# Kernel tuning notes

Measured on AMD Instinct MI355X. Metric: run time of the kernel, lower is better.

The kernel has to match this reference:

```python
import jax, jax.numpy as jnp
import numpy as np

P = 8            # window_size
SHIFT = P // 2   # cyclic shift for 'SW' type
HEADS = 6        # input_dim // head_dim = 192 // 32
HD = 32          # head_dim
C = 192          # input_dim
OUT = 192        # output_dim
SCALE = HD ** (-0.5)


def setup_inputs() -> dict:
    key = jax.random.key(0)
    ks = jax.random.split(key, 8)
    f = lambda k, sh: jax.random.normal(k, sh, dtype=jnp.float32)
    return {
        "x": f(ks[0], (2, 256, 256, C)),
        "b": f(ks[1], (2, 256, 256, C)),
        "w_qkv": f(ks[2], (3 * C, C)) * 0.02,
        "b_qkv": jnp.zeros((3 * C,), jnp.float32),
        "w_qkv_b": f(ks[3], (3 * C, C)) * 0.02,
        "b_qkv_b": jnp.zeros((3 * C,), jnp.float32),
        "rel_params": f(ks[4], (HEADS, 2 * P - 1, 2 * P - 1)) * 0.02,
        "w_out": f(ks[5], (OUT, C)) * 0.02,
        "b_out": jnp.zeros((OUT,), jnp.float32),
    }


def _rel_bias(rel_params):
    # gathered relative position bias: (HEADS, P*P, P*P)
    cord = np.array([[i, j] for i in range(P) for j in range(P)])
    rel = cord[:, None, :] - cord[None, :, :] + P - 1
    return rel_params[:, rel[:, :, 0], rel[:, :, 1]]


def _shift_mask(hw, ww):
    # bool mask (nw, P*P, P*P); True -> -inf before softmax
    m = np.zeros((hw, ww, P, P, P, P), dtype=bool)
    s = P - SHIFT
    m[-1, :, :s, :, s:, :] = True
    m[-1, :, s:, :, :s, :] = True
    m[:, -1, :, :s, :, s:] = True
    m[:, -1, :, s:, :, :s] = True
    return jnp.asarray(m.reshape(hw * ww, P * P, P * P))


def reference(x, b, w_qkv, b_qkv, w_qkv_b, b_qkv_b, rel_params, w_out, b_out):
    # cyclic shift (type != 'W')
    x = jnp.roll(x, (-SHIFT, -SHIFT), axis=(1, 2))
    b = jnp.roll(b, (-SHIFT, -SHIFT), axis=(1, 2))
    B, H, W, c = x.shape
    hw, ww = H // P, W // P
    nw, pp = hw * ww, P * P

    def windows(t):  # [B,H,W,C] -> [B,nw,pp,C]
        return t.reshape(B, hw, P, ww, P, c).transpose(0, 1, 3, 2, 4, 5).reshape(B, nw, pp, c)

    xw, bw = windows(x), windows(b)

    def qkv(t, w, bb):  # returns q,k,v each (HEADS, B, nw, pp, HD)
        e = (t @ w.T + bb).reshape(B, nw, pp, 3 * HEADS, HD)
        e = jnp.moveaxis(e, 3, 0)
        return e[:HEADS], e[HEADS:2 * HEADS], e[2 * HEADS:]

    _, k, v = qkv(xw, w_qkv, b_qkv)
    q_b, _, _ = qkv(bw, w_qkv_b, b_qkv_b)

    sim = jnp.einsum('hbwpc,hbwqc->hbwpq', q_b, k) * SCALE
    sim = sim + _rel_bias(rel_params)[:, None, None]
    mask = _shift_mask(hw, ww)  # (nw, pp, pp)
    sim = jnp.where(mask[None, None], -jnp.inf, sim)
    probs = jax.nn.softmax(sim, axis=-1)
    out = jnp.einsum('hbwij,hbwjc->hbwic', probs, v)
    out = jnp.moveaxis(out, 0, 3).reshape(B, nw, pp, HEADS * HD)
    out = out @ w_out.T + b_out
    out = out.reshape(B, hw, ww, P, P, OUT).transpose(0, 1, 3, 2, 4, 5).reshape(B, H, W, OUT)
    return jnp.roll(out, (SHIFT, SHIFT), axis=(1, 2))
```

## Files before the change

### kernel.cpp

```cpp
#include <hip/hip_runtime.h>


#define NHEADS 6
#define CDIM 192
#define IMG 256
#define SHIFTV 4
#define SCALE_F 0.17677669529663687f

typedef __attribute__((ext_vector_type(8))) _Float16 h8;
typedef __attribute__((ext_vector_type(4))) _Float16 h4;
typedef __attribute__((ext_vector_type(4))) float f4;

#define MFMA(a, b, c) __builtin_amdgcn_mfma_f32_16x16x32_f16((a), (b), (c), 0, 0, 0)

__global__ void prep_weights(const float* __restrict__ wqb,
                             const float* __restrict__ wqkv,
                             const float* __restrict__ wout,
                             _Float16* __restrict__ dst)
{
    const int i = blockIdx.x * 256 + threadIdx.x;
    const int m = i / 36864, r = i - m * 36864;
    float v;
    if (m == 0)      v = wqb[r];
    else if (m == 1) v = wqkv[36864 + r];
    else if (m == 2) v = wqkv[73728 + r];
    else             v = wout[r];
    dst[i] = (_Float16)v;
}

__global__ void prep_table(const float* __restrict__ rel, float* __restrict__ tab)
{
    const int i = blockIdx.x * 256 + threadIdx.x;
    const int k = i & 63, q = (i >> 6) & 63;
    const int th = i >> 12;
    const int h = th % 6, ty = th / 6;
    const int pr = q >> 3, pc = q & 7, qr = k >> 3, qc = k & 7;
    const bool msk = ((ty & 1) && ((pr < 4) != (qr < 4))) ||
                     ((ty & 2) && ((pc < 4) != (qc < 4)));
    const float bias = rel[h * 225 + (pr - qr + 7) * 15 + (pc - qc + 7)];
    tab[i] = msk ? -1e30f : bias;
}

__global__ __launch_bounds__(256, 3)
void wmca_mfma(const float* __restrict__ x, const float* __restrict__ bten,
               const float* __restrict__ b_qkv, const float* __restrict__ b_qkv_b,
               const float* __restrict__ b_out,
               const _Float16* __restrict__ wh, const float* __restrict__ tab,
               float* __restrict__ out)
{
    __shared__ _Float16 sX[64 * 200];
    __shared__ _Float16 sQ[64 * 40];
    __shared__ _Float16 sK[64 * 40];
    __shared__ _Float16 sVt[32 * 72];
    __shared__ _Float16 sP[64 * 72];

    const int t = threadIdx.x;
    const int w = t >> 6, l = t & 63, g = l >> 4, c16 = l & 15;

    const int wid = blockIdx.x;
    const int bi = wid >> 10, whi = (wid >> 5) & 31, wwi = wid & 31;
    const int ty = ((whi == 31) ? 1 : 0) | ((wwi == 31) ? 2 : 0);

    {
        const int rr = t >> 2, part = t & 3;
        const int pr = rr >> 3, pc = rr & 7;
        const int ho = (whi * 8 + pr + SHIFTV) & 255;
        const int wo = (wwi * 8 + pc + SHIFTV) & 255;
        const float4* xs = (const float4*)(x + ((bi * IMG + ho) * IMG + wo) * CDIM);
        _Float16* dX = sX + rr * 200;
#pragma unroll
        for (int i = 0; i < 12; ++i) {
            const int q4 = part + 4 * i;
            const float4 v = xs[q4];
            h4 hv; hv[0] = (_Float16)v.x; hv[1] = (_Float16)v.y;
                   hv[2] = (_Float16)v.z; hv[3] = (_Float16)v.w;
            *(h4*)(dX + 4 * q4) = hv;
        }
    }

    const int tokA = 16 * w + c16;
    const int prA = tokA >> 3, pcA = tokA & 7;
    const int hoA = (whi * 8 + prA + SHIFTV) & 255;
    const int woA = (wwi * 8 + pcA + SHIFTV) & 255;
    const float* bA = bten + ((bi * IMG + hoA) * IMG + woA) * CDIM;

    h8 aQ[6];
#pragma unroll
    for (int ks = 0; ks < 6; ++ks) {
        const float4 f0 = *(const float4*)(bA + ks * 32 + 8 * g);
        const float4 f1 = *(const float4*)(bA + ks * 32 + 8 * g + 4);
        h8 a;
        a[0] = (_Float16)f0.x; a[1] = (_Float16)f0.y;
        a[2] = (_Float16)f0.z; a[3] = (_Float16)f0.w;
        a[4] = (_Float16)f1.x; a[5] = (_Float16)f1.y;
        a[6] = (_Float16)f1.z; a[7] = (_Float16)f1.w;
        aQ[ks] = a;
    }

    f4 pacc[12];
#pragma unroll
    for (int nt = 0; nt < 12; ++nt) {
        const float bo = b_out[16 * nt + c16];
        pacc[nt] = (f4){bo, bo, bo, bo};
    }

    const _Float16* Wq = wh;
    const _Float16* Wk = wh + 36864;
    const _Float16* Wv = wh + 2 * 36864;
    const _Float16* Wo = wh + 3 * 36864;
    const int vm = w & 1, vn = w >> 1;

    __syncthreads();

    for (int h = 0; h < NHEADS; ++h) {
        {
            const float b0 = b_qkv_b[h * 32 + c16];
            const float b1 = b_qkv_b[h * 32 + 16 + c16];
            f4 a0 = {b0, b0, b0, b0}, a1 = {b1, b1, b1, b1};
            const _Float16* wr0 = Wq + (h * 32 + c16) * 192 + 8 * g;
            const _Float16* wr1 = wr0 + 16 * 192;
#pragma unroll
            for (int ks = 0; ks < 6; ++ks) {
                a0 = MFMA(aQ[ks], *(const h8*)(wr0 + ks * 32), a0);
                a1 = MFMA(aQ[ks], *(const h8*)(wr1 + ks * 32), a1);
            }
#pragma unroll
            for (int rg = 0; rg < 4; ++rg) {
                sQ[(16 * w + 4 * g + rg) * 40 + c16]      = (_Float16)(a0[rg] * SCALE_F);
                sQ[(16 * w + 4 * g + rg) * 40 + 16 + c16] = (_Float16)(a1[rg] * SCALE_F);
            }
        }
        {
            const float b0 = b_qkv[CDIM + h * 32 + c16];
            const float b1 = b_qkv[CDIM + h * 32 + 16 + c16];
            f4 a0 = {b0, b0, b0, b0}, a1 = {b1, b1, b1, b1};
            const _Float16* xr = sX + (16 * w + c16) * 200 + 8 * g;
            const _Float16* wr0 = Wk + (h * 32 + c16) * 192 + 8 * g;
            const _Float16* wr1 = wr0 + 16 * 192;
#pragma unroll
            for (int ks = 0; ks < 6; ++ks) {
                const h8 a = *(const h8*)(xr + ks * 32);
                a0 = MFMA(a, *(const h8*)(wr0 + ks * 32), a0);
                a1 = MFMA(a, *(const h8*)(wr1 + ks * 32), a1);
            }
#pragma unroll
            for (int rg = 0; rg < 4; ++rg) {
                sK[(16 * w + 4 * g + rg) * 40 + c16]      = (_Float16)a0[rg];
                sK[(16 * w + 4 * g + rg) * 40 + 16 + c16] = (_Float16)a1[rg];
            }
        }
        {
            const float4 bv = *(const float4*)(b_qkv + 2 * CDIM + h * 32 + 16 * vm + 4 * g);
            f4 a0 = {bv.x, bv.y, bv.z, bv.w};
            f4 a1 = a0;
            const _Float16* wr = Wv + (h * 32 + 16 * vm + c16) * 192 + 8 * g;
            const _Float16* x0 = sX + (32 * vn + c16) * 200 + 8 * g;
            const _Float16* x1 = x0 + 16 * 200;
#pragma unroll
            for (int ks = 0; ks < 6; ++ks) {
                const h8 a = *(const h8*)(wr + ks * 32);
                a0 = MFMA(a, *(const h8*)(x0 + ks * 32), a0);
                a1 = MFMA(a, *(const h8*)(x1 + ks * 32), a1);
            }
#pragma unroll
            for (int rg = 0; rg < 4; ++rg) {
                sVt[(16 * vm + 4 * g + rg) * 72 + 32 * vn + c16]      = (_Float16)a0[rg];
                sVt[(16 * vm + 4 * g + rg) * 72 + 32 * vn + 16 + c16] = (_Float16)a1[rg];
            }
        }
        __syncthreads();

        {
            const float* tr = tab + ((ty * 6 + h) << 12) + (16 * w + 4 * g) * 64 + c16;
            f4 s0, s1, s2, s3;
#pragma unroll
            for (int rg = 0; rg < 4; ++rg) {
                s0[rg] = tr[rg * 64];
                s1[rg] = tr[rg * 64 + 16];
                s2[rg] = tr[rg * 64 + 32];
                s3[rg] = tr[rg * 64 + 48];
            }
            const h8 qa = *(const h8*)(sQ + (16 * w + c16) * 40 + 8 * g);
            s0 = MFMA(qa, *(const h8*)(sK + c16 * 40 + 8 * g), s0);
            s1 = MFMA(qa, *(const h8*)(sK + (16 + c16) * 40 + 8 * g), s1);
            s2 = MFMA(qa, *(const h8*)(sK + (32 + c16) * 40 + 8 * g), s2);
            s3 = MFMA(qa, *(const h8*)(sK + (48 + c16) * 40 + 8 * g), s3);
#pragma unroll
            for (int rg = 0; rg < 4; ++rg) {
                float mx = fmaxf(fmaxf(s0[rg], s1[rg]), fmaxf(s2[rg], s3[rg]));
                mx = fmaxf(mx, __shfl_xor(mx, 1));
                mx = fmaxf(mx, __shfl_xor(mx, 2));
                mx = fmaxf(mx, __shfl_xor(mx, 4));
                mx = fmaxf(mx, __shfl_xor(mx, 8));
                const float e0 = __expf(s0[rg] - mx);
                const float e1 = __expf(s1[rg] - mx);
                const float e2 = __expf(s2[rg] - mx);
                const float e3 = __expf(s3[rg] - mx);
                float sm = e0 + e1 + e2 + e3;
                sm += __shfl_xor(sm, 1);
                sm += __shfl_xor(sm, 2);
                sm += __shfl_xor(sm, 4);
                sm += __shfl_xor(sm, 8);
                const float inv = 1.0f / sm;
                _Float16* prow = sP + (16 * w + 4 * g + rg) * 72 + c16;
                prow[0]  = (_Float16)(e0 * inv);
                prow[16] = (_Float16)(e1 * inv);
                prow[32] = (_Float16)(e2 * inv);
                prow[48] = (_Float16)(e3 * inv);
            }
        }

        {
            const h8 pa0 = *(const h8*)(sP + (16 * w + c16) * 72 + 8 * g);
            const h8 pa1 = *(const h8*)(sP + (16 * w + c16) * 72 + 32 + 8 * g);
            f4 o0 = {0.f, 0.f, 0.f, 0.f}, o1 = o0;
            o0 = MFMA(pa0, *(const h8*)(sVt + c16 * 72 + 8 * g), o0);
            o0 = MFMA(pa1, *(const h8*)(sVt + c16 * 72 + 32 + 8 * g), o0);
            o1 = MFMA(pa0, *(const h8*)(sVt + (16 + c16) * 72 + 8 * g), o1);
            o1 = MFMA(pa1, *(const h8*)(sVt + (16 + c16) * 72 + 32 + 8 * g), o1);
#pragma unroll
            for (int rg = 0; rg < 4; ++rg) {
                sQ[(16 * w + 4 * g + rg) * 40 + c16]      = (_Float16)o0[rg];
                sQ[(16 * w + 4 * g + rg) * 40 + 16 + c16] = (_Float16)o1[rg];
            }
        }
        __syncthreads();

        {
            const h8 oa = *(const h8*)(sQ + (16 * w + c16) * 40 + 8 * g);
            const _Float16* wr = Wo + c16 * 192 + h * 32 + 8 * g;
#pragma unroll
            for (int nt = 0; nt < 12; ++nt)
                pacc[nt] = MFMA(oa, *(const h8*)(wr + nt * 16 * 192), pacc[nt]);
        }
    }

#pragma unroll
    for (int rg = 0; rg < 4; ++rg) {
        const int token = 16 * w + 4 * g + rg;
        const int pr = token >> 3, pc = token & 7;
        const int ho = (whi * 8 + pr + SHIFTV) & 255;
        const int wo = (wwi * 8 + pc + SHIFTV) & 255;
        float* po = out + ((bi * IMG + ho) * IMG + wo) * CDIM + c16;
#pragma unroll
        for (int nt = 0; nt < 12; ++nt)
            po[16 * nt] = pacc[nt][rg];
    }
}

extern "C" void kernel_launch(void* const* d_in, const int* in_sizes, int n_in,
                              void* d_out, int out_size, void* d_ws, size_t ws_size,
                              hipStream_t stream)
{
    const float* x       = (const float*)d_in[0];
    const float* b       = (const float*)d_in[1];
    const float* w_qkv   = (const float*)d_in[2];
    const float* b_qkv   = (const float*)d_in[3];
    const float* w_qkv_b = (const float*)d_in[4];
    const float* b_qkv_b = (const float*)d_in[5];
    const float* rel     = (const float*)d_in[6];
    const float* w_out   = (const float*)d_in[7];
    const float* b_out   = (const float*)d_in[8];
    float* out = (float*)d_out;

    _Float16* wh = (_Float16*)d_ws;
    float* tab = (float*)((char*)d_ws + 294912);

    prep_weights<<<576, 256, 0, stream>>>(w_qkv_b, w_qkv, w_out, wh);
    prep_table<<<384, 256, 0, stream>>>(rel, tab);
    wmca_mfma<<<2048, 256, 0, stream>>>(x, b, b_qkv, b_qkv_b, b_out, wh, tab, out);
}
```

Before: 514.2 us.

## Assign one wavefront per head and drop per-head block barriers

```diff
diff --git a/kernel.cpp b/kernel.cpp
--- a/kernel.cpp
+++ b/kernel.cpp
@@ -1,17 +1,26 @@
 #include <hip/hip_runtime.h>
 
 
-#define NHEADS 6
-#define CDIM 192
 #define IMG 256
 #define SHIFTV 4
 #define SCALE_F 0.17677669529663687f
 
 typedef __attribute__((ext_vector_type(8))) _Float16 h8;
-typedef __attribute__((ext_vector_type(4))) _Float16 h4;
 typedef __attribute__((ext_vector_type(4))) float f4;
 
 #define MFMA(a, b, c) __builtin_amdgcn_mfma_f32_16x16x32_f16((a), (b), (c), 0, 0, 0)
+
+__device__ __forceinline__ h8 cvt8(const float* __restrict__ p)
+{
+    const float4 f0 = *(const float4*)p;
+    const float4 f1 = *(const float4*)(p + 4);
+    h8 a;
+    a[0] = (_Float16)f0.x; a[1] = (_Float16)f0.y;
+    a[2] = (_Float16)f0.z; a[3] = (_Float16)f0.w;
+    a[4] = (_Float16)f1.x; a[5] = (_Float16)f1.y;
+    a[6] = (_Float16)f1.z; a[7] = (_Float16)f1.w;
+    return a;
+}
 
 __global__ void prep_weights(const float* __restrict__ wqb,
                              const float* __restrict__ wqkv,
@@ -41,211 +50,261 @@
     tab[i] = msk ? -1e30f : bias;
 }
 
-__global__ __launch_bounds__(256, 3)
-void wmca_mfma(const float* __restrict__ x, const float* __restrict__ bten,
-               const float* __restrict__ b_qkv, const float* __restrict__ b_qkv_b,
-               const float* __restrict__ b_out,
-               const _Float16* __restrict__ wh, const float* __restrict__ tab,
-               float* __restrict__ out)
-{
-    __shared__ _Float16 sX[64 * 200];
-    __shared__ _Float16 sQ[64 * 40];
-    __shared__ _Float16 sK[64 * 40];
-    __shared__ _Float16 sVt[32 * 72];
-    __shared__ _Float16 sP[64 * 72];
+__global__ __launch_bounds__(384, 3)
+void wmca_hpw(const float* __restrict__ x, const float* __restrict__ bten,
+              const float* __restrict__ b_qkv, const float* __restrict__ b_qkv_b,
+              const float* __restrict__ b_out,
+              const _Float16* __restrict__ wh, const float* __restrict__ tab,
+              float* __restrict__ out)
+{
+    __shared__ _Float16 sPool[6 * 64 * 72];
 
     const int t = threadIdx.x;
-    const int w = t >> 6, l = t & 63, g = l >> 4, c16 = l & 15;
+    const int w = t >> 6;
+    const int l = t & 63, g = l >> 4, c16 = l & 15;
 
     const int wid = blockIdx.x;
     const int bi = wid >> 10, whi = (wid >> 5) & 31, wwi = wid & 31;
     const int ty = ((whi == 31) ? 1 : 0) | ((wwi == 31) ? 2 : 0);
 
-    {
-        const int rr = t >> 2, part = t & 3;
-        const int pr = rr >> 3, pc = rr & 7;
-        const int ho = (whi * 8 + pr + SHIFTV) & 255;
-        const int wo = (wwi * 8 + pc + SHIFTV) & 255;
-        const float4* xs = (const float4*)(x + ((bi * IMG + ho) * IMG + wo) * CDIM);
-        _Float16* dX = sX + rr * 200;
-#pragma unroll
-        for (int i = 0; i < 12; ++i) {
-            const int q4 = part + 4 * i;
-            const float4 v = xs[q4];
-            h4 hv; hv[0] = (_Float16)v.x; hv[1] = (_Float16)v.y;
-                   hv[2] = (_Float16)v.z; hv[3] = (_Float16)v.w;
-            *(h4*)(dX + 4 * q4) = hv;
-        }
-    }
-
-    const int tokA = 16 * w + c16;
-    const int prA = tokA >> 3, pcA = tokA & 7;
-    const int hoA = (whi * 8 + prA + SHIFTV) & 255;
-    const int woA = (wwi * 8 + pcA + SHIFTV) & 255;
-    const float* bA = bten + ((bi * IMG + hoA) * IMG + woA) * CDIM;
-
-    h8 aQ[6];
-#pragma unroll
-    for (int ks = 0; ks < 6; ++ks) {
-        const float4 f0 = *(const float4*)(bA + ks * 32 + 8 * g);
-        const float4 f1 = *(const float4*)(bA + ks * 32 + 8 * g + 4);
-        h8 a;
-        a[0] = (_Float16)f0.x; a[1] = (_Float16)f0.y;
-        a[2] = (_Float16)f0.z; a[3] = (_Float16)f0.w;
-        a[4] = (_Float16)f1.x; a[5] = (_Float16)f1.y;
-        a[6] = (_Float16)f1.z; a[7] = (_Float16)f1.w;
-        aQ[ks] = a;
-    }
-
-    f4 pacc[12];
-#pragma unroll
-    for (int nt = 0; nt < 12; ++nt) {
-        const float bo = b_out[16 * nt + c16];
-        pacc[nt] = (f4){bo, bo, bo, bo};
+    _Float16* bounce = sPool + w * (64 * 72);
+
+    const float* xR[4]; const float* bR[4];
+#pragma unroll
+    for (int m = 0; m < 4; ++m) {
+        const int tok = 16 * m + c16;
+        const int ho = (whi * 8 + (tok >> 3) + SHIFTV) & 255;
+        const int wo = (wwi * 8 + (tok & 7) + SHIFTV) & 255;
+        const int base = ((bi * IMG + ho) * IMG + wo) * 192;
+        xR[m] = x + base; bR[m] = bten + base;
     }
 
     const _Float16* Wq = wh;
     const _Float16* Wk = wh + 36864;
     const _Float16* Wv = wh + 2 * 36864;
     const _Float16* Wo = wh + 3 * 36864;
-    const int vm = w & 1, vn = w >> 1;
+
+    {
+        f4 qacc[4][2];
+#pragma unroll
+        for (int n = 0; n < 2; ++n) {
+            const float bb = b_qkv_b[w * 32 + 16 * n + c16];
+#pragma unroll
+            for (int m = 0; m < 4; ++m) qacc[m][n] = (f4){bb, bb, bb, bb};
+        }
+#pragma unroll
+        for (int ks = 0; ks < 6; ++ks) {
+            h8 wB0 = *(const h8*)(Wq + (w * 32 + c16) * 192 + 32 * ks + 8 * g);
+            h8 wB1 = *(const h8*)(Wq + (w * 32 + 16 + c16) * 192 + 32 * ks + 8 * g);
+#pragma unroll
+            for (int m = 0; m < 4; ++m) {
+                const h8 aB = cvt8(bR[m] + 32 * ks + 8 * g);
+                qacc[m][0] = MFMA(aB, wB0, qacc[m][0]);
+                qacc[m][1] = MFMA(aB, wB1, qacc[m][1]);
+            }
+        }
+#pragma unroll
+        for (int m = 0; m < 4; ++m)
+#pragma unroll
+            for (int n = 0; n < 2; ++n)
+#pragma unroll
+                for (int rg = 0; rg < 4; ++rg)
+                    bounce[(16 * m + 4 * g + rg) * 72 + 16 * n + c16] =
+                        (_Float16)(qacc[m][n][rg] * SCALE_F);
+    }
+    h8 qa[4];
+#pragma unroll
+    for (int m = 0; m < 4; ++m)
+        qa[m] = *(const h8*)(bounce + (16 * m + c16) * 72 + 8 * g);
+
+    {
+        f4 kacc[4][2];
+#pragma unroll
+        for (int n = 0; n < 2; ++n) {
+            const float bb = b_qkv[192 + w * 32 + 16 * n + c16];
+#pragma unroll
+            for (int m = 0; m < 4; ++m) kacc[m][n] = (f4){bb, bb, bb, bb};
+        }
+#pragma unroll
+        for (int ks = 0; ks < 6; ++ks) {
+            h8 wB0 = *(const h8*)(Wk + (w * 32 + c16) * 192 + 32 * ks + 8 * g);
+            h8 wB1 = *(const h8*)(Wk + (w * 32 + 16 + c16) * 192 + 32 * ks + 8 * g);
+#pragma unroll
+            for (int m = 0; m < 4; ++m) {
+                const h8 aB = cvt8(xR[m] + 32 * ks + 8 * g);
+                kacc[m][0] = MFMA(aB, wB0, kacc[m][0]);
+                kacc[m][1] = MFMA(aB, wB1, kacc[m][1]);
+            }
+        }
+#pragma unroll
+        for (int m = 0; m < 4; ++m)
+#pragma unroll
+            for (int n = 0; n < 2; ++n)
+#pragma unroll
+                for (int rg = 0; rg < 4; ++rg)
+                    bounce[(16 * m + 4 * g + rg) * 72 + 16 * n + c16] =
+                        (_Float16)kacc[m][n][rg];
+    }
+    h8 kb[4];
+#pragma unroll
+    for (int n = 0; n < 4; ++n)
+        kb[n] = *(const h8*)(bounce + (16 * n + c16) * 72 + 8 * g);
+
+    {
+        f4 vacc[2][4];
+#pragma unroll
+        for (int mv = 0; mv < 2; ++mv) {
+            const float4 bv = *(const float4*)(b_qkv + 384 + w * 32 + 16 * mv + 4 * g);
+#pragma unroll
+            for (int n = 0; n < 4; ++n) vacc[mv][n] = (f4){bv.x, bv.y, bv.z, bv.w};
+        }
+#pragma unroll
+        for (int ks = 0; ks < 6; ++ks) {
+            h8 wA0 = *(const h8*)(Wv + (w * 32 + c16) * 192 + 32 * ks + 8 * g);
+            h8 wA1 = *(const h8*)(Wv + (w * 32 + 16 + c16) * 192 + 32 * ks + 8 * g);
+#pragma unroll
+            for (int n = 0; n < 4; ++n) {
+                const h8 xv = cvt8(xR[n] + 32 * ks + 8 * g);
+                vacc[0][n] = MFMA(wA0, xv, vacc[0][n]);
+                vacc[1][n] = MFMA(wA1, xv, vacc[1][n]);
+            }
+        }
+#pragma unroll
+        for (int mv = 0; mv < 2; ++mv)
+#pragma unroll
+            for (int n = 0; n < 4; ++n)
+#pragma unroll
+                for (int rg = 0; rg < 4; ++rg)
+                    bounce[(16 * mv + 4 * g + rg) * 72 + 16 * n + c16] =
+                        (_Float16)vacc[mv][n][rg];
+    }
+    h8 vb[2][2];
+#pragma unroll
+    for (int ks2 = 0; ks2 < 2; ++ks2)
+#pragma unroll
+        for (int n = 0; n < 2; ++n)
+            vb[ks2][n] = *(const h8*)(bounce + (16 * n + c16) * 72 + 32 * ks2 + 8 * g);
+
+    f4 s[4][4];
+    {
+        const float* tb = tab + ((ty * 6 + w) << 12);
+#pragma unroll
+        for (int m = 0; m < 4; ++m)
+#pragma unroll
+            for (int n = 0; n < 4; ++n)
+#pragma unroll
+                for (int rg = 0; rg < 4; ++rg)
+                    s[m][n][rg] = tb[(16 * m + 4 * g + rg) * 64 + 16 * n + c16];
+#pragma unroll
+        for (int m = 0; m < 4; ++m)
+#pragma unroll
+            for (int n = 0; n < 4; ++n)
+                s[m][n] = MFMA(qa[m], kb[n], s[m][n]);
+    }
+
+    f4 inv4[4];
+#pragma unroll
+    for (int m = 0; m < 4; ++m) {
+#pragma unroll
+        for (int rg = 0; rg < 4; ++rg) {
+            float mx = fmaxf(fmaxf(s[m][0][rg], s[m][1][rg]),
+                             fmaxf(s[m][2][rg], s[m][3][rg]));
+            mx = fmaxf(mx, __shfl_xor(mx, 1));
+            mx = fmaxf(mx, __shfl_xor(mx, 2));
+            mx = fmaxf(mx, __shfl_xor(mx, 4));
+            mx = fmaxf(mx, __shfl_xor(mx, 8));
+            const float e0 = __expf(s[m][0][rg] - mx);
+            const float e1 = __expf(s[m][1][rg] - mx);
+            const float e2 = __expf(s[m][2][rg] - mx);
+            const float e3 = __expf(s[m][3][rg] - mx);
+            float sm = e0 + e1 + e2 + e3;
+            sm += __shfl_xor(sm, 1);
+            sm += __shfl_xor(sm, 2);
+            sm += __shfl_xor(sm, 4);
+            sm += __shfl_xor(sm, 8);
+            inv4[m][rg] = 1.0f / sm;
+            _Float16* prow = bounce + (16 * m + 4 * g + rg) * 72 + c16;
+            prow[0]  = (_Float16)e0;
+            prow[16] = (_Float16)e1;
+            prow[32] = (_Float16)e2;
+            prow[48] = (_Float16)e3;
+        }
+    }
+
+    f4 o[4][2];
+    {
+        h8 pa[4][2];
+#pragma unroll
+        for (int m = 0; m < 4; ++m)
+#pragma unroll
+            for (int ks2 = 0; ks2 < 2; ++ks2)
+                pa[m][ks2] = *(const h8*)(bounce + (16 * m + c16) * 72 + 32 * ks2 + 8 * g);
+#pragma unroll
+        for (int m = 0; m < 4; ++m)
+#pragma unroll
+            for (int n = 0; n < 2; ++n) {
+                f4 acc = (f4){0.f, 0.f, 0.f, 0.f};
+                acc = MFMA(pa[m][0], vb[0][n], acc);
+                acc = MFMA(pa[m][1], vb[1][n], acc);
+                o[m][n] = acc;
+            }
+#pragma unroll
+        for (int m = 0; m < 4; ++m)
+#pragma unroll
+            for (int n = 0; n < 2; ++n)
+#pragma unroll
+                for (int rg = 0; rg < 4; ++rg)
+                    o[m][n][rg] *= inv4[m][rg];
+    }
 
     __syncthreads();
 
-    for (int h = 0; h < NHEADS; ++h) {
-        {
-            const float b0 = b_qkv_b[h * 32 + c16];
-            const float b1 = b_qkv_b[h * 32 + 16 + c16];
-            f4 a0 = {b0, b0, b0, b0}, a1 = {b1, b1, b1, b1};
-            const _Float16* wr0 = Wq + (h * 32 + c16) * 192 + 8 * g;
-            const _Float16* wr1 = wr0 + 16 * 192;
-#pragma unroll
-            for (int ks = 0; ks < 6; ++ks) {
-                a0 = MFMA(aQ[ks], *(const h8*)(wr0 + ks * 32), a0);
-                a1 = MFMA(aQ[ks], *(const h8*)(wr1 + ks * 32), a1);
-            }
-#pragma unroll
-            for (int rg = 0; rg < 4; ++rg) {
-                sQ[(16 * w + 4 * g + rg) * 40 + c16]      = (_Float16)(a0[rg] * SCALE_F);
-                sQ[(16 * w + 4 * g + rg) * 40 + 16 + c16] = (_Float16)(a1[rg] * SCALE_F);
-            }
-        }
-        {
-            const float b0 = b_qkv[CDIM + h * 32 + c16];
-            const float b1 = b_qkv[CDIM + h * 32 + 16 + c16];
-            f4 a0 = {b0, b0, b0, b0}, a1 = {b1, b1, b1, b1};
-            const _Float16* xr = sX + (16 * w + c16) * 200 + 8 * g;
-            const _Float16* wr0 = Wk + (h * 32 + c16) * 192 + 8 * g;
-            const _Float16* wr1 = wr0 + 16 * 192;
-#pragma unroll
-            for (int ks = 0; ks < 6; ++ks) {
-                const h8 a = *(const h8*)(xr + ks * 32);
-                a0 = MFMA(a, *(const h8*)(wr0 + ks * 32), a0);
-                a1 = MFMA(a, *(const h8*)(wr1 + ks * 32), a1);
-            }
-#pragma unroll
-            for (int rg = 0; rg < 4; ++rg) {
-                sK[(16 * w + 4 * g + rg) * 40 + c16]      = (_Float16)a0[rg];
-                sK[(16 * w + 4 * g + rg) * 40 + 16 + c16] = (_Float16)a1[rg];
-            }
-        }
-        {
-            const float4 bv = *(const float4*)(b_qkv + 2 * CDIM + h * 32 + 16 * vm + 4 * g);
-            f4 a0 = {bv.x, bv.y, bv.z, bv.w};
-            f4 a1 = a0;
-            const _Float16* wr = Wv + (h * 32 + 16 * vm + c16) * 192 + 8 * g;
-            const _Float16* x0 = sX + (32 * vn + c16) * 200 + 8 * g;
-            const _Float16* x1 = x0 + 16 * 200;
-#pragma unroll
-            for (int ks = 0; ks < 6; ++ks) {
-                const h8 a = *(const h8*)(wr + ks * 32);
-                a0 = MFMA(a, *(const h8*)(x0 + ks * 32), a0);
-                a1 = MFMA(a, *(const h8*)(x1 + ks * 32), a1);
-            }
-#pragma unroll
-            for (int rg = 0; rg < 4; ++rg) {
-                sVt[(16 * vm + 4 * g + rg) * 72 + 32 * vn + c16]      = (_Float16)a0[rg];
-                sVt[(16 * vm + 4 * g + rg) * 72 + 32 * vn + 16 + c16] = (_Float16)a1[rg];
-            }
-        }
-        __syncthreads();
-
-        {
-            const float* tr = tab + ((ty * 6 + h) << 12) + (16 * w + 4 * g) * 64 + c16;
-            f4 s0, s1, s2, s3;
-#pragma unroll
-            for (int rg = 0; rg < 4; ++rg) {
-                s0[rg] = tr[rg * 64];
-                s1[rg] = tr[rg * 64 + 16];
-                s2[rg] = tr[rg * 64 + 32];
-                s3[rg] = tr[rg * 64 + 48];
-            }
-            const h8 qa = *(const h8*)(sQ + (16 * w + c16) * 40 + 8 * g);
-            s0 = MFMA(qa, *(const h8*)(sK + c16 * 40 + 8 * g), s0);
-            s1 = MFMA(qa, *(const h8*)(sK + (16 + c16) * 40 + 8 * g), s1);
-            s2 = MFMA(qa, *(const h8*)(sK + (32 + c16) * 40 + 8 * g), s2);
-            s3 = MFMA(qa, *(const h8*)(sK + (48 + c16) * 40 + 8 * g), s3);
-#pragma unroll
-            for (int rg = 0; rg < 4; ++rg) {
-                float mx = fmaxf(fmaxf(s0[rg], s1[rg]), fmaxf(s2[rg], s3[rg]));
-                mx = fmaxf(mx, __shfl_xor(mx, 1));
-                mx = fmaxf(mx, __shfl_xor(mx, 2));
-                mx = fmaxf(mx, __shfl_xor(mx, 4));
-                mx = fmaxf(mx, __shfl_xor(mx, 8));
-                const float e0 = __expf(s0[rg] - mx);
-                const float e1 = __expf(s1[rg] - mx);
-                const float e2 = __expf(s2[rg] - mx);
-                const float e3 = __expf(s3[rg] - mx);
-                float sm = e0 + e1 + e2 + e3;
-                sm += __shfl_xor(sm, 1);
-                sm += __shfl_xor(sm, 2);
-                sm += __shfl_xor(sm, 4);
-                sm += __shfl_xor(sm, 8);
-                const float inv = 1.0f / sm;
-                _Float16* prow = sP + (16 * w + 4 * g + rg) * 72 + c16;
-                prow[0]  = (_Float16)(e0 * inv);
-                prow[16] = (_Float16)(e1 * inv);
-                prow[32] = (_Float16)(e2 * inv);
-                prow[48] = (_Float16)(e3 * inv);
-            }
-        }
-
-        {
-            const h8 pa0 = *(const h8*)(sP + (16 * w + c16) * 72 + 8 * g);
-            const h8 pa1 = *(const h8*)(sP + (16 * w + c16) * 72 + 32 + 8 * g);
-            f4 o0 = {0.f, 0.f, 0.f, 0.f}, o1 = o0;
-            o0 = MFMA(pa0, *(const h8*)(sVt + c16 * 72 + 8 * g), o0);
-            o0 = MFMA(pa1, *(const h8*)(sVt + c16 * 72 + 32 + 8 * g), o0);
-            o1 = MFMA(pa0, *(const h8*)(sVt + (16 + c16) * 72 + 8 * g), o1);
-            o1 = MFMA(pa1, *(const h8*)(sVt + (16 + c16) * 72 + 32 + 8 * g), o1);
-#pragma unroll
-            for (int rg = 0; rg < 4; ++rg) {
-                sQ[(16 * w + 4 * g + rg) * 40 + c16]      = (_Float16)o0[rg];
-                sQ[(16 * w + 4 * g + rg) * 40 + 16 + c16] = (_Float16)o1[rg];
-            }
-        }
-        __syncthreads();
-
-        {
-            const h8 oa = *(const h8*)(sQ + (16 * w + c16) * 40 + 8 * g);
-            const _Float16* wr = Wo + c16 * 192 + h * 32 + 8 * g;
-#pragma unroll
-            for (int nt = 0; nt < 12; ++nt)
-                pacc[nt] = MFMA(oa, *(const h8*)(wr + nt * 16 * 192), pacc[nt]);
-        }
-    }
-
-#pragma unroll
-    for (int rg = 0; rg < 4; ++rg) {
-        const int token = 16 * w + 4 * g + rg;
-        const int pr = token >> 3, pc = token & 7;
-        const int ho = (whi * 8 + pr + SHIFTV) & 255;
-        const int wo = (wwi * 8 + pc + SHIFTV) & 255;
-        float* po = out + ((bi * IMG + ho) * IMG + wo) * CDIM + c16;
-#pragma unroll
-        for (int nt = 0; nt < 12; ++nt)
-            po[16 * nt] = pacc[nt][rg];
-    }
+    {
+        _Float16* sO = sPool;
+#pragma unroll
+        for (int m = 0; m < 4; ++m)
+#pragma unroll
+            for (int n = 0; n < 2; ++n)
+#pragma unroll
+                for (int rg = 0; rg < 4; ++rg)
+                    sO[(16 * m + 4 * g + rg) * 200 + w * 32 + 16 * n + c16] =
+                        (_Float16)o[m][n][rg];
+    }
+    __syncthreads();
+
+    f4 pacc[4][2];
+#pragma unroll
+    for (int n = 0; n < 2; ++n) {
+        const float bo = b_out[32 * w + 16 * n + c16];
+#pragma unroll
+        for (int m = 0; m < 4; ++m) pacc[m][n] = (f4){bo, bo, bo, bo};
+    }
+    {
+        const _Float16* sO = sPool;
+#pragma unroll
+        for (int ks = 0; ks < 6; ++ks) {
+            h8 wB0 = *(const h8*)(Wo + (32 * w + c16) * 192 + 32 * ks + 8 * g);
+            h8 wB1 = *(const h8*)(Wo + (32 * w + 16 + c16) * 192 + 32 * ks + 8 * g);
+#pragma unroll
+            for (int m = 0; m < 4; ++m) {
+                const h8 oa = *(const h8*)(sO + (16 * m + c16) * 200 + 32 * ks + 8 * g);
+                pacc[m][0] = MFMA(oa, wB0, pacc[m][0]);
+                pacc[m][1] = MFMA(oa, wB1, pacc[m][1]);
+            }
+        }
+    }
+
+#pragma unroll
+    for (int m = 0; m < 4; ++m)
+#pragma unroll
+        for (int rg = 0; rg < 4; ++rg) {
+            const int tok = 16 * m + 4 * g + rg;
+            const int ho = (whi * 8 + (tok >> 3) + SHIFTV) & 255;
+            const int wo = (wwi * 8 + (tok & 7) + SHIFTV) & 255;
+            float* po = out + ((bi * IMG + ho) * IMG + wo) * 192 + 32 * w + c16;
+            po[0]  = pacc[m][0][rg];
+            po[16] = pacc[m][1][rg];
+        }
 }
 
 extern "C" void kernel_launch(void* const* d_in, const int* in_sizes, int n_in,
@@ -268,5 +327,5 @@
 
     prep_weights<<<576, 256, 0, stream>>>(w_qkv_b, w_qkv, w_out, wh);
     prep_table<<<384, 256, 0, stream>>>(rel, tab);
-    wmca_mfma<<<2048, 256, 0, stream>>>(x, b, b_qkv, b_qkv_b, b_out, wh, tab, out);
-}
+    wmca_hpw<<<2048, 384, 0, stream>>>(x, b, b_qkv, b_qkv_b, b_out, wh, tab, out);
+}
```

Result: slower. 888.8 us (+72.8%).
